# Performance work log

Measured on AMD Instinct MI355X. Metric: run time of the kernel, lower is better.

Reference implementation:

```python
import jax, jax.numpy as jnp
import numpy as np

# FrictionConfig constants (chosen in init_kwargs)
K_STEPS = 4
ETA = 0.1
ETA_DECAY = 0.9
MU_MAX = 10.0
SMOOTH_LAMBDA = 0.1
RADIUS = 8
B, S, H = 4, 2048, 1024
INNER = max(H // 2, 32)  # 512


def _build_window_edges(length, radius):
    chunks = []
    for d in range(1, radius + 1):
        i = np.arange(length - d, dtype=np.int32)
        chunks.append(np.stack([i, i + d], axis=1))
    return np.concatenate(chunks, axis=0)  # [E, 2]


def setup_inputs() -> dict:
    key = jax.random.key(0)
    ks = jax.random.split(key, 8)
    hidden = jax.random.normal(ks[0], (B, S, H), dtype=jnp.float32)
    attention_mask = jnp.ones((B, S), dtype=jnp.int32)
    edges = jnp.asarray(_build_window_edges(S, RADIUS))
    # edge_mlp: Linear(2, INNER) -> GELU -> Linear(INNER, 1)
    W1 = jax.random.normal(ks[1], (2, INNER), dtype=jnp.float32) * (1.0 / np.sqrt(2))
    b1 = jnp.zeros((INNER,), dtype=jnp.float32)
    W2 = jax.random.normal(ks[2], (INNER, 1), dtype=jnp.float32) * (1.0 / np.sqrt(INNER))
    b2 = jnp.zeros((1,), dtype=jnp.float32)
    # q_proj: Linear(H, H)
    Wq = jax.random.normal(ks[3], (H, H), dtype=jnp.float32) * (1.0 / np.sqrt(H))
    bq = jnp.zeros((H,), dtype=jnp.float32)
    # LayerNorm
    gamma = jnp.ones((H,), dtype=jnp.float32)
    beta = jnp.zeros((H,), dtype=jnp.float32)
    return {"hidden": hidden, "attention_mask": attention_mask, "edges": edges,
            "Wq": Wq, "bq": bq, "W1": W1, "b1": b1, "W2": W2, "b2": b2,
            "gamma": gamma, "beta": beta}


def _edge_weights(h, ei, ej, W1, b1, W2, b2):
    hi = h[ei]  # [E, H]
    hj = h[ej]
    diff = hi - hj
    dist = jnp.linalg.norm(diff, axis=-1, keepdims=True)           # [E, 1]
    ni = jnp.maximum(jnp.linalg.norm(hi, axis=-1), 1e-6)
    nj = jnp.maximum(jnp.linalg.norm(hj, axis=-1), 1e-6)
    cos = (jnp.sum(hi * hj, axis=-1) / (ni * nj))[:, None]         # [E, 1]
    feats = jnp.concatenate([dist, cos], axis=-1)                  # [E, 2]
    z = jax.nn.gelu(feats @ W1 + b1, approximate=False) @ W2 + b2  # [E, 1]
    return jax.nn.softplus(z) + 1e-5


def _laplacian(h, ei, ej, mu):
    n = h.shape[0]
    weighted = mu * (h[ei] - h[ej])  # [E, H]
    # normalize_laplacian = True
    w = mu[:, 0]
    deg = jnp.zeros((n,), h.dtype).at[ei].add(w).at[ej].add(w)
    inv_sqrt = jnp.maximum(deg, 1e-6) ** -0.5
    weighted = weighted * (inv_sqrt[ei] * inv_sqrt[ej])[:, None]
    lap = jnp.zeros_like(h).at[ei].add(weighted).at[ej].add(-weighted)
    return lap


def _smooth(s):
    left = jnp.concatenate([s[:1], s[:-1]], axis=0)
    right = jnp.concatenate([s[1:], s[-1:]], axis=0)
    return s - SMOOTH_LAMBDA * (2.0 * s - left - right)


def _layernorm(x, gamma, beta):
    m = x.mean(axis=-1, keepdims=True)
    v = x.var(axis=-1, keepdims=True)
    return (x - m) * jax.lax.rsqrt(v + 1e-5) * gamma + beta


def _run_single(h, ei, ej, Wq, bq, W1, b1, W2, b2, gamma, beta):
    q = h @ Wq + bq
    state = h
    mu = None
    for step in range(K_STEPS):
        mu = _edge_weights(state, ei, ej, W1, b1, W2, b2)  # recompute_mu=True
        mu = jnp.minimum(mu, MU_MAX)
        lap = _laplacian(state, ei, ej, mu)
        eta = ETA * (ETA_DECAY ** step)
        state = state - eta * (lap - q)
        state = _smooth(state)
    out = _layernorm(state + h, gamma, beta)
    diffs = state[ei] - state[ej]
    energy = 0.5 * jnp.sum(mu[:, 0] * jnp.sum(diffs * diffs, axis=-1))
    return out, energy


def reference(hidden, attention_mask, edges, Wq, bq, W1, b1, W2, b2, gamma, beta):
    # All masks are full-length, so edges are identical across batch and
    # the outer Python batch loop vectorizes to a vmap.
    ei, ej = edges[:, 0], edges[:, 1]
    outputs, energy = jax.vmap(
        lambda h: _run_single(h, ei, ej, Wq, bq, W1, b1, W2, b2, gamma, beta)
    )(hidden)
    return outputs, energy
```

## Files before the change

### kernel.cpp

```cpp
#include <hip/hip_runtime.h>

#define BB 4
#define SS 2048
#define HH 1024
#define TQ 32
#define TU 32
#define CW 256

typedef unsigned short u16;
typedef __bf16 bf16x8 __attribute__((ext_vector_type(8)));
typedef float f32x4 __attribute__((ext_vector_type(4)));

__device__ __forceinline__ float b2f(u16 u){
  union { unsigned int i; float f; } v; v.i = ((unsigned int)u) << 16; return v.f;
}
__device__ __forceinline__ u16 f2b(float f){
  union { float f; unsigned int i; } v; v.f = f;
  unsigned int x = v.i;
  return (u16)((x + 0x7fffu + ((x >> 16) & 1u)) >> 16);
}
__device__ __forceinline__ float4 u4f(ushort4 v){
  float4 o; o.x = b2f(v.x); o.y = b2f(v.y); o.z = b2f(v.z); o.w = b2f(v.w); return o;
}
__device__ __forceinline__ ushort4 f4u(float4 v){
  ushort4 o; o.x = f2b(v.x); o.y = f2b(v.y); o.z = f2b(v.z); o.w = f2b(v.w); return o;
}
__device__ __forceinline__ float wave_sum(float v){
  #pragma unroll
  for(int m = 32; m > 0; m >>= 1) v += __shfl_xor(v, m);
  return v;
}
__device__ __forceinline__ float pread(const void* p, int i, int f){
  return f ? b2f(((const u16*)p)[i]) : ((const float*)p)[i];
}
__device__ __forceinline__ void gload16(const void* g, void* l){
  __builtin_amdgcn_global_load_lds((const __attribute__((address_space(1))) unsigned int*)g,
                                   (__attribute__((address_space(3))) unsigned int*)l, 16, 0, 0);
}
__device__ __forceinline__ float fast_gelu(float z){
  float x  = z * 0.70710678118654752f;
  float ax = fabsf(x);
  float t  = __builtin_amdgcn_rcpf(fmaf(0.3275911f, ax, 1.f));
  float poly = ((((1.061405429f*t - 1.453152027f)*t + 1.421413741f)*t
                 - 0.284496736f)*t + 0.254829592f)*t;
  float er = fmaf(-poly, __expf(-ax*ax), 1.f);
  er = (x < 0.f) ? -er : er;
  return 0.5f*z*(1.f + er);
}

__global__ __launch_bounds__(256) void k_params(const void* bq, const void* W1, const void* b1,
                                                const void* W2, const void* b2, const void* gm,
                                                const void* bt, float* bqc, float* W1c, float* b1c,
                                                float* W2c, float* b2c, float* gmc, float* btc,
                                                int* flagp){
  __shared__ int sf;
  if(threadIdx.x == 0){
    int f = (((const u16*)gm)[0] == 0x3F80u) ? 1 : 0;
    sf = f; *flagp = f;
  }
  __syncthreads();
  int f = sf, t = threadIdx.x;
  for(int i = t; i < 1024; i += 256) bqc[i] = pread(bq, i, f);
  for(int i = t; i < 1024; i += 256) W1c[i] = pread(W1, i, f);
  for(int i = t; i <  512; i += 256) b1c[i] = pread(b1, i, f);
  for(int i = t; i <  512; i += 256) W2c[i] = pread(W2, i, f);
  if(t == 0) b2c[0] = pread(b2, 0, f);
  for(int i = t; i < 1024; i += 256) gmc[i] = pread(gm, i, f);
  for(int i = t; i < 1024; i += 256) btc[i] = pread(bt, i, f);
}

__global__ __launch_bounds__(256) void k_cvt(const void* h, u16* s, const int* flagp){
  int f = *flagp;
  size_t i4 = (size_t)blockIdx.x*256 + threadIdx.x;
  if(f){
    ((ushort4*)s)[i4] = ((const ushort4*)h)[i4];
  } else {
    float4 v = ((const float4*)h)[i4];
    ((ushort4*)s)[i4] = f4u(v);
  }
}

__global__ __launch_bounds__(256) void k_transpose(const void* W, u16* __restrict__ Wt,
                                                   const int* flagp){
  int f = *flagp;
  __shared__ u16 t[32][33];
  int bx = blockIdx.x, by = blockIdx.y;
  int tx = threadIdx.x, ty = threadIdx.y;
  #pragma unroll
  for(int r = 0; r < 32; r += 8){
    int idx = (by*32 + ty + r)*HH + bx*32 + tx;
    float v = f ? b2f(((const u16*)W)[idx]) : ((const float*)W)[idx];
    t[ty + r][tx] = f2b(v);
  }
  __syncthreads();
  #pragma unroll
  for(int r = 0; r < 32; r += 8)
    Wt[(size_t)(bx*32 + ty + r)*HH + by*32 + tx] = t[tx][ty + r];
}

__global__ __launch_bounds__(256) void k_qgemm(const u16* __restrict__ A, const u16* __restrict__ Wt,
                                               const float* __restrict__ bqc, u16* __restrict__ q){
  __shared__ u16 lA[128*32];
  __shared__ u16 lB[128*32];
  int m0 = blockIdx.x*128, n0 = blockIdx.y*128;
  int tid  = threadIdx.x;
  int wave = tid >> 6, lane = tid & 63;
  int wm = (wave >> 1)*64, wn = (wave & 1)*64;
  int quad = lane >> 4, l16 = lane & 15;
  int srow = tid >> 2;
  int scol = (tid & 3)*8;

  f32x4 acc[4][4];
  #pragma unroll
  for(int i = 0; i < 4; i++)
    #pragma unroll
    for(int j = 0; j < 4; j++) acc[i][j] = (f32x4){0.f,0.f,0.f,0.f};

  for(int k0 = 0; k0 < HH; k0 += 32){
    __syncthreads();
    gload16(A  + (size_t)(m0 + srow     )*HH + k0 + scol, &lA[ srow     *32 + scol]);
    gload16(A  + (size_t)(m0 + srow + 64)*HH + k0 + scol, &lA[(srow+64) *32 + scol]);
    gload16(Wt + (size_t)(n0 + srow     )*HH + k0 + scol, &lB[ srow     *32 + scol]);
    gload16(Wt + (size_t)(n0 + srow + 64)*HH + k0 + scol, &lB[(srow+64) *32 + scol]);
    __syncthreads();
    bf16x8 af[4];
    #pragma unroll
    for(int mt = 0; mt < 4; mt++)
      af[mt] = *(const bf16x8*)&lA[(wm + mt*16 + l16)*32 + quad*8];
    #pragma unroll
    for(int nt = 0; nt < 4; nt++){
      bf16x8 bf = *(const bf16x8*)&lB[(wn + nt*16 + l16)*32 + quad*8];
      #pragma unroll
      for(int mt = 0; mt < 4; mt++)
        acc[mt][nt] = __builtin_amdgcn_mfma_f32_16x16x32_bf16(af[mt], bf, acc[mt][nt], 0, 0, 0);
    }
  }
  #pragma unroll
  for(int nt = 0; nt < 4; nt++){
    int col = n0 + wn + nt*16 + l16;
    float bqv = bqc[col];
    #pragma unroll
    for(int mt = 0; mt < 4; mt++){
      #pragma unroll
      for(int r = 0; r < 4; r++){
        int row = m0 + wm + mt*16 + quad*4 + r;
        q[(size_t)row*HH + col] = f2b(acc[mt][nt][r] + bqv);
      }
    }
  }
}

__global__ __launch_bounds__(512) void k_gram_mu(const u16* __restrict__ s,
                                                 const float* __restrict__ W1c, const float* __restrict__ b1c,
                                                 const float* __restrict__ W2c, const float* __restrict__ b2c,
                                                 float* __restrict__ mu){
  __shared__ float Gband[40*9];
  __shared__ float4 wpk[512];
  int b = blockIdx.y, i0 = blockIdx.x*TQ;
  int tid = threadIdx.x, wave = tid >> 6, lane = tid & 63;

  if(tid < 512) wpk[tid] = make_float4(W1c[tid], W1c[512+tid], b1c[tid], W2c[tid]);

  if(wave < 4){
    int ti = wave >> 1;
    int tj = (wave + 1) >> 1;
    int quad = lane >> 4, l16 = lane & 15;
    int ra = i0 + ti*16 + l16; if(ra > SS-1) ra = SS-1;
    int rb = i0 + tj*16 + l16; if(rb > SS-1) rb = SS-1;
    const u16* ar = s + ((size_t)b*SS + ra)*HH + quad*8;
    const u16* br = s + ((size_t)b*SS + rb)*HH + quad*8;
    f32x4 acc = (f32x4){0.f,0.f,0.f,0.f};
    #pragma unroll 8
    for(int k0 = 0; k0 < HH; k0 += 32){
      bf16x8 af = *(const bf16x8*)(ar + k0);
      bf16x8 bf = *(const bf16x8*)(br + k0);
      acc = __builtin_amdgcn_mfma_f32_16x16x32_bf16(af, bf, acc, 0, 0, 0);
    }
    #pragma unroll
    for(int r = 0; r < 4; r++){
      int gr = ti*16 + quad*4 + r;
      int dd = tj*16 + l16 - gr;
      if(dd >= 0 && dd <= 8) Gband[gr*9 + dd] = acc[r];
    }
  } else {
    for(int rr = wave - 4; rr < 8; rr += 4){
      int r = 32 + rr;
      int row = i0 + r; if(row > SS-1) row = SS-1;
      const ushort4* rp = (const ushort4*)(s + ((size_t)b*SS + row)*HH);
      float a = 0.f;
      #pragma unroll
      for(int c = 0; c < 4; c++){
        float4 v = u4f(rp[lane + 64*c]);
        a += v.x*v.x + v.y*v.y + v.z*v.z + v.w*v.w;
      }
      a = wave_sum(a);
      if(lane == 0) Gband[r*9] = a;
    }
  }
  __syncthreads();

  int e = tid >> 1, h = tid & 1;
  int d = (e >> 5) + 1, k = e & 31;
  bool valid = (i0 + k + d) < SS;
  float gii = Gband[k*9], gjj = Gband[(k+d)*9], gij = Gband[k*9 + d];
  float dist = sqrtf(fmaxf(gii + gjj - 2.f*gij, 0.f));
  float ni = fmaxf(sqrtf(gii), 1e-6f);
  float nj = fmaxf(sqrtf(gjj), 1e-6f);
  float cosv = gij * __builtin_amdgcn_rcpf(ni * nj);
  float acc = 0.f;
  const float4* wp = &wpk[h*256];
  #pragma unroll 4
  for(int j0 = 0; j0 < 256; j0++){
    float4 wv = wp[j0];
    float z1 = fmaf(dist, wv.x, fmaf(cosv, wv.y, wv.z));
    acc = fmaf(fast_gelu(z1), wv.w, acc);
  }
  acc += __shfl_xor(acc, 1);
  if(h == 0 && valid){
    float z  = acc + b2c[0];
    float sp = fmaxf(z, 0.f) + __logf(1.f + __expf(-fabsf(z)));
    mu[((size_t)b*8 + (d-1))*SS + (i0 + k)] = fminf(sp + 1e-5f, 10.0f);
  }
}

__global__ __launch_bounds__(256) void k_upsm(const u16* __restrict__ sIn, u16* __restrict__ sOut,
                                              const u16* __restrict__ q, const float* __restrict__ mu,
                                              float eta){
  __shared__ u16 st[50*CW];
  __shared__ u16 up[34*CW];
  __shared__ float invsS[50];
  __shared__ float muS[58*8];
  int i0 = blockIdx.x*TU, c0 = blockIdx.y*CW, b = blockIdx.z;
  int tid = threadIdx.x;

  for(int idx = tid; idx < 58*8; idx += 256){
    int ir = idx >> 3, d = (idx & 7) + 1;
    int i = i0 - 17 + ir;
    float v = 0.f;
    if(i >= 0 && i + d < SS) v = mu[((size_t)b*8 + d-1)*SS + i];
    muS[idx] = v;
  }
  for(int idx = tid; idx < 50*(CW/4); idx += 256){
    int r = idx / (CW/4), cc = idx % (CW/4);
    int i = i0 - 9 + r;
    ushort4 v = {0,0,0,0};
    if(i >= 0 && i < SS) v = *(const ushort4*)(sIn + ((size_t)b*SS + i)*HH + c0 + cc*4);
    ((ushort4*)st)[idx] = v;
  }
  __syncthreads();
  if(tid < 50){
    int ir = tid + 8;
    float deg = 0.f;
    #pragma unroll
    for(int d = 1; d <= 8; d++){
      deg += muS[ir*8 + d-1];
      deg += muS[(ir-d)*8 + d-1];
    }
    invsS[tid] = 1.0f / sqrtf(fmaxf(deg, 1e-6f));
  }
  __syncthreads();

  int rq = tid >> 6, lane = tid & 63;
  for(int jr = 0; jr < 9; jr++){
    int r = rq + jr*4;
    if(r >= 34) break;
    int i = i0 - 1 + r;
    if(i < 0 || i >= SS) continue;
    int sr = r + 8, vr = r + 8, mr = r + 16;
    float inv_i = invsS[vr];
    float4 si = u4f(((const ushort4*)(st + (size_t)sr*CW))[lane]);
    float A = 0.f;
    float4 acc = {0.f,0.f,0.f,0.f};
    #pragma unroll
    for(int d = 1; d <= 8; d++){
      float cR = muS[mr*8 + d-1]     * inv_i        * invsS[vr+d];
      float cL = muS[(mr-d)*8 + d-1] * invsS[vr-d]  * inv_i;
      A += cR + cL;
      float4 vR = u4f(((const ushort4*)(st + (size_t)(sr+d)*CW))[lane]);
      float4 vL = u4f(((const ushort4*)(st + (size_t)(sr-d)*CW))[lane]);
      acc.x -= cR*vR.x + cL*vL.x; acc.y -= cR*vR.y + cL*vL.y;
      acc.z -= cR*vR.z + cL*vL.z; acc.w -= cR*vR.w + cL*vL.w;
    }
    acc.x += A*si.x; acc.y += A*si.y; acc.z += A*si.z; acc.w += A*si.w;
    float4 qv = u4f(*(const ushort4*)(q + ((size_t)b*SS + i)*HH + c0 + lane*4));
    float4 o;
    o.x = si.x - eta*(acc.x - qv.x);
    o.y = si.y - eta*(acc.y - qv.y);
    o.z = si.z - eta*(acc.z - qv.z);
    o.w = si.w - eta*(acc.w - qv.w);
    ((ushort4*)(up + (size_t)r*CW))[lane] = f4u(o);
  }
  __syncthreads();
  for(int js = 0; js < 8; js++){
    int rr = rq + js*4;
    int i = i0 + rr;
    int ur = rr + 1;
    float4 c  = u4f(((const ushort4*)(up + (size_t)ur*CW))[lane]);
    float4 l  = (i > 0)      ? u4f(((const ushort4*)(up + (size_t)(ur-1)*CW))[lane]) : c;
    float4 r4 = (i < SS-1)   ? u4f(((const ushort4*)(up + (size_t)(ur+1)*CW))[lane]) : c;
    float4 o;
    o.x = c.x - 0.1f*(2.f*c.x - l.x - r4.x);
    o.y = c.y - 0.1f*(2.f*c.y - l.y - r4.y);
    o.z = c.z - 0.1f*(2.f*c.z - l.z - r4.z);
    o.w = c.w - 0.1f*(2.f*c.w - l.w - r4.w);
    *(ushort4*)(sOut + ((size_t)b*SS + i)*HH + c0 + lane*4) = f4u(o);
  }
}

__global__ __launch_bounds__(256) void k_out(const u16* __restrict__ sA, const void* __restrict__ hraw,
                                             const float* __restrict__ gmc, const float* __restrict__ btc,
                                             void* __restrict__ outp, const int* flagp){
  int f = *flagp;
  int b = blockIdx.x >> 11, i = blockIdx.x & (SS-1);
  int tid = threadIdx.x;
  size_t row = (size_t)b*SS + i;
  float4 sv = u4f(((const ushort4*)(sA + row*HH))[tid]);
  float4 hv;
  if(f) hv = u4f(((const ushort4*)((const u16*)hraw + row*HH))[tid]);
  else  hv = ((const float4*)((const float*)hraw + row*HH))[tid];
  float x0 = sv.x + hv.x, x1 = sv.y + hv.y, x2 = sv.z + hv.z, x3 = sv.w + hv.w;

  __shared__ float sh[4];
  int wv = tid >> 6, lane = tid & 63;
  float lsum = wave_sum(x0 + x1 + x2 + x3);
  if(lane == 0) sh[wv] = lsum;
  __syncthreads();
  float mean = (sh[0] + sh[1] + sh[2] + sh[3]) * (1.f/HH);
  __syncthreads();
  float d0 = x0-mean, d1 = x1-mean, d2 = x2-mean, d3 = x3-mean;
  float lsq = wave_sum(d0*d0 + d1*d1 + d2*d2 + d3*d3);
  if(lane == 0) sh[wv] = lsq;
  __syncthreads();
  float var = (sh[0] + sh[1] + sh[2] + sh[3]) * (1.f/HH);
  float sc = 1.0f / sqrtf(var + 1e-5f);

  int col = tid*4;
  float4 o;
  o.x = d0*sc*gmc[col+0] + btc[col+0];
  o.y = d1*sc*gmc[col+1] + btc[col+1];
  o.z = d2*sc*gmc[col+2] + btc[col+2];
  o.w = d3*sc*gmc[col+3] + btc[col+3];
  if(f) ((ushort4*)((u16*)outp + row*HH))[tid] = f4u(o);
  else  ((float4*)((float*)outp + row*HH))[tid] = o;
}

__global__ __launch_bounds__(512) void k_energy(const u16* __restrict__ s, const float* __restrict__ mu,
                                                float* __restrict__ partials){
  __shared__ float Gband[40*9];
  __shared__ float wacc[8];
  int b = blockIdx.y, i0 = blockIdx.x*TQ;
  int tid = threadIdx.x, wave = tid >> 6, lane = tid & 63;

  if(wave < 4){
    int ti = wave >> 1;
    int tj = (wave + 1) >> 1;
    int quad = lane >> 4, l16 = lane & 15;
    int ra = i0 + ti*16 + l16; if(ra > SS-1) ra = SS-1;
    int rb = i0 + tj*16 + l16; if(rb > SS-1) rb = SS-1;
    const u16* ar = s + ((size_t)b*SS + ra)*HH + quad*8;
    const u16* br = s + ((size_t)b*SS + rb)*HH + quad*8;
    f32x4 acc = (f32x4){0.f,0.f,0.f,0.f};
    #pragma unroll 8
    for(int k0 = 0; k0 < HH; k0 += 32){
      bf16x8 af = *(const bf16x8*)(ar + k0);
      bf16x8 bf = *(const bf16x8*)(br + k0);
      acc = __builtin_amdgcn_mfma_f32_16x16x32_bf16(af, bf, acc, 0, 0, 0);
    }
    #pragma unroll
    for(int r = 0; r < 4; r++){
      int gr = ti*16 + quad*4 + r;
      int dd = tj*16 + l16 - gr;
      if(dd >= 0 && dd <= 8) Gband[gr*9 + dd] = acc[r];
    }
  } else {
    for(int rr = wave - 4; rr < 8; rr += 4){
      int r = 32 + rr;
      int row = i0 + r; if(row > SS-1) row = SS-1;
      const ushort4* rp = (const ushort4*)(s + ((size_t)b*SS + row)*HH);
      float a = 0.f;
      #pragma unroll
      for(int c = 0; c < 4; c++){
        float4 v = u4f(rp[lane + 64*c]);
        a += v.x*v.x + v.y*v.y + v.z*v.z + v.w*v.w;
      }
      a = wave_sum(a);
      if(lane == 0) Gband[r*9] = a;
    }
  }
  __syncthreads();

  int d = wave + 1;
  int k = lane;
  float esum = 0.f;
  if(k < 32 && (i0 + k + d) < SS){
    float d2 = fmaxf(Gband[k*9] + Gband[(k+d)*9] - 2.f*Gband[k*9 + d], 0.f);
    esum = mu[((size_t)b*8 + (d-1))*SS + (i0 + k)] * d2;
  }
  esum = wave_sum(esum);
  if(lane == 0) wacc[wave] = esum;
  __syncthreads();
  if(tid == 0){
    float t = 0.f;
    #pragma unroll
    for(int w2 = 0; w2 < 8; w2++) t += wacc[w2];
    partials[(size_t)b*64 + blockIdx.x] = t;
  }
}

__global__ __launch_bounds__(64) void k_efinal(const float* __restrict__ partials, void* __restrict__ outp,
                                               const int* flagp){
  int f = *flagp;
  int b = blockIdx.x;
  float sacc = partials[(size_t)b*64 + threadIdx.x];
  sacc = wave_sum(sacc);
  if(threadIdx.x == 0){
    float e = 0.5f * sacc;
    if(f) ((u16*)outp)[(size_t)BB*SS*HH + b] = f2b(e);
    else  ((float*)outp)[(size_t)BB*SS*HH + b] = e;
  }
}

extern "C" void kernel_launch(void* const* d_in, const int* in_sizes, int n_in,
                              void* d_out, int out_size, void* d_ws, size_t ws_size,
                              hipStream_t stream) {
  const void* hidden = d_in[0];
  const void* Wq  = d_in[3];
  const void* bq  = d_in[4];
  const void* W1  = d_in[5];
  const void* b1  = d_in[6];
  const void* W2  = d_in[7];
  const void* b2v = d_in[8];
  const void* gamma = d_in[9];
  const void* beta  = d_in[10];

  char* w = (char*)d_ws;
  u16*   q   = (u16*)w;   w += (size_t)BB*SS*HH*2;
  u16*   sA  = (u16*)w;   w += (size_t)BB*SS*HH*2;
  u16*   Wt  = (u16*)w;   w += (size_t)HH*HH*2;
  float* mu  = (float*)w; w += (size_t)BB*8*SS*4;
  float* partials = (float*)w; w += (size_t)BB*64*4;
  float* bqc = (float*)w; w += 1024*4;
  float* W1c = (float*)w; w += 1024*4;
  float* b1c = (float*)w; w += 512*4;
  float* W2c = (float*)w; w += 512*4;
  float* b2c = (float*)w; w += 4;
  float* gmc = (float*)w; w += 1024*4;
  float* btc = (float*)w; w += 1024*4;
  int*   flagp = (int*)w; w += 4;
  u16* sB = (u16*)d_out;

  k_params   <<<1, 256, 0, stream>>>(bq, W1, b1, W2, b2v, gamma, beta,
                                     bqc, W1c, b1c, W2c, b2c, gmc, btc, flagp);
  k_cvt      <<<(BB*SS*HH/4)/256, 256, 0, stream>>>(hidden, sA, flagp);
  k_transpose<<<dim3(HH/32, HH/32), dim3(32,8), 0, stream>>>(Wq, Wt, flagp);
  k_qgemm    <<<dim3(BB*SS/128, HH/128), 256, 0, stream>>>(sA, Wt, bqc, q);

  const float etas[4] = {0.1f, 0.09f, 0.081f, 0.0729f};
  for(int step = 0; step < 4; step++){
    const u16* cur = (step & 1) ? sB : sA;
    u16*       nxt = (step & 1) ? sA : sB;
    k_gram_mu<<<dim3(SS/TQ, BB), 512, 0, stream>>>(cur, W1c, b1c, W2c, b2c, mu);
    k_upsm   <<<dim3(SS/TU, HH/CW, BB), 256, 0, stream>>>(cur, nxt, q, mu, etas[step]);
  }
  k_out   <<<BB*SS, 256, 0, stream>>>(sA, hidden, gmc, btc, d_out, flagp);
  k_energy<<<dim3(SS/TQ, BB), 512, 0, stream>>>(sA, mu, partials);
  k_efinal<<<BB, 64, 0, stream>>>(partials, d_out, flagp);
}
```

Before: 406.0 us.

## Fuse setup kernels, split gram_mu edges, register-pipeline upsm smoothing, fuse energy reduction

Merges the param, convert and transpose kernels into one launch and folds the final energy reduction into k_energy with atomics and a last-block counter. This removes three kernel launches. k_gram_mu now splits the 8 distances across two blocks and uses 4 lanes per edge. It folds the 1/sqrt2 scale into the weights and simplifies the GELU algebra. k_upsm drops the shared up buffer and applies the 3-tap smoothing from a rolling register window. That saves LDS and a barrier but recomputes two halo rows per wave group.

```diff
diff --git a/kernel.cpp b/kernel.cpp
--- a/kernel.cpp
+++ b/kernel.cpp
@@ -33,69 +33,56 @@
 __device__ __forceinline__ float pread(const void* p, int i, int f){
   return f ? b2f(((const u16*)p)[i]) : ((const float*)p)[i];
 }
+__device__ __forceinline__ int dflag(const void* gm){
+  return (((const u16*)gm)[0] == 0x3F80u) ? 1 : 0;
+}
 __device__ __forceinline__ void gload16(const void* g, void* l){
   __builtin_amdgcn_global_load_lds((const __attribute__((address_space(1))) unsigned int*)g,
                                    (__attribute__((address_space(3))) unsigned int*)l, 16, 0, 0);
 }
-__device__ __forceinline__ float fast_gelu(float z){
-  float x  = z * 0.70710678118654752f;
-  float ax = fabsf(x);
-  float t  = __builtin_amdgcn_rcpf(fmaf(0.3275911f, ax, 1.f));
-  float poly = ((((1.061405429f*t - 1.453152027f)*t + 1.421413741f)*t
-                 - 0.284496736f)*t + 0.254829592f)*t;
-  float er = fmaf(-poly, __expf(-ax*ax), 1.f);
-  er = (x < 0.f) ? -er : er;
-  return 0.5f*z*(1.f + er);
-}
-
-__global__ __launch_bounds__(256) void k_params(const void* bq, const void* W1, const void* b1,
-                                                const void* W2, const void* b2, const void* gm,
-                                                const void* bt, float* bqc, float* W1c, float* b1c,
-                                                float* W2c, float* b2c, float* gmc, float* btc,
-                                                int* flagp){
-  __shared__ int sf;
-  if(threadIdx.x == 0){
-    int f = (((const u16*)gm)[0] == 0x3F80u) ? 1 : 0;
-    sf = f; *flagp = f;
-  }
-  __syncthreads();
-  int f = sf, t = threadIdx.x;
-  for(int i = t; i < 1024; i += 256) bqc[i] = pread(bq, i, f);
-  for(int i = t; i < 1024; i += 256) W1c[i] = pread(W1, i, f);
-  for(int i = t; i <  512; i += 256) b1c[i] = pread(b1, i, f);
-  for(int i = t; i <  512; i += 256) W2c[i] = pread(W2, i, f);
-  if(t == 0) b2c[0] = pread(b2, 0, f);
-  for(int i = t; i < 1024; i += 256) gmc[i] = pread(gm, i, f);
-  for(int i = t; i < 1024; i += 256) btc[i] = pread(bt, i, f);
-}
-
-__global__ __launch_bounds__(256) void k_cvt(const void* h, u16* s, const int* flagp){
-  int f = *flagp;
-  size_t i4 = (size_t)blockIdx.x*256 + threadIdx.x;
-  if(f){
-    ((ushort4*)s)[i4] = ((const ushort4*)h)[i4];
+
+__global__ __launch_bounds__(256) void k_setup(const void* hidden, u16* __restrict__ s,
+                                               const void* Wq, u16* __restrict__ Wt,
+                                               const void* bq, const void* W1, const void* b1,
+                                               const void* W2, const void* b2, const void* gm,
+                                               const void* bt,
+                                               float* bqc, float* W1c, float* b1c, float* W2c,
+                                               float* b2c, float* gmc, float* btc,
+                                               float* partials, int* ecnt){
+  __shared__ u16 t[32][33];
+  int f = dflag(gm);
+  int bid = blockIdx.x, tid = threadIdx.x;
+  if(bid < 8192){
+    size_t i4 = (size_t)bid*256 + tid;
+    if(f){
+      ((ushort4*)s)[i4] = ((const ushort4*)hidden)[i4];
+    } else {
+      ((ushort4*)s)[i4] = f4u(((const float4*)hidden)[i4]);
+    }
+  } else if(bid < 8192 + 1024){
+    int bi = bid - 8192;
+    int bx = bi & 31, by = bi >> 5;
+    int tx = tid & 31, ty = tid >> 5;
+    #pragma unroll
+    for(int r = 0; r < 32; r += 8){
+      int idx = (by*32 + ty + r)*HH + bx*32 + tx;
+      float v = f ? b2f(((const u16*)Wq)[idx]) : ((const float*)Wq)[idx];
+      t[ty + r][tx] = f2b(v);
+    }
+    __syncthreads();
+    #pragma unroll
+    for(int r = 0; r < 32; r += 8)
+      Wt[(size_t)(bx*32 + ty + r)*HH + by*32 + tx] = t[tx][ty + r];
   } else {
-    float4 v = ((const float4*)h)[i4];
-    ((ushort4*)s)[i4] = f4u(v);
-  }
-}
-
-__global__ __launch_bounds__(256) void k_transpose(const void* W, u16* __restrict__ Wt,
-                                                   const int* flagp){
-  int f = *flagp;
-  __shared__ u16 t[32][33];
-  int bx = blockIdx.x, by = blockIdx.y;
-  int tx = threadIdx.x, ty = threadIdx.y;
-  #pragma unroll
-  for(int r = 0; r < 32; r += 8){
-    int idx = (by*32 + ty + r)*HH + bx*32 + tx;
-    float v = f ? b2f(((const u16*)W)[idx]) : ((const float*)W)[idx];
-    t[ty + r][tx] = f2b(v);
-  }
-  __syncthreads();
-  #pragma unroll
-  for(int r = 0; r < 32; r += 8)
-    Wt[(size_t)(bx*32 + ty + r)*HH + by*32 + tx] = t[tx][ty + r];
+    for(int i = tid; i < 1024; i += 256) bqc[i] = pread(bq, i, f);
+    for(int i = tid; i < 1024; i += 256) W1c[i] = pread(W1, i, f);
+    for(int i = tid; i <  512; i += 256) b1c[i] = pread(b1, i, f);
+    for(int i = tid; i <  512; i += 256) W2c[i] = pread(W2, i, f);
+    if(tid == 0) b2c[0] = pread(b2, 0, f);
+    for(int i = tid; i < 1024; i += 256) gmc[i] = pread(gm, i, f);
+    for(int i = tid; i < 1024; i += 256) btc[i] = pread(bt, i, f);
+    if(tid < BB){ partials[tid] = 0.f; ecnt[tid] = 0; }
+  }
 }
 
 __global__ __launch_bounds__(256) void k_qgemm(const u16* __restrict__ A, const u16* __restrict__ Wt,
@@ -156,10 +143,13 @@
                                                  float* __restrict__ mu){
   __shared__ float Gband[40*9];
   __shared__ float4 wpk[512];
-  int b = blockIdx.y, i0 = blockIdx.x*TQ;
+  int b = blockIdx.z, i0 = blockIdx.x*TQ;
   int tid = threadIdx.x, wave = tid >> 6, lane = tid & 63;
 
-  if(tid < 512) wpk[tid] = make_float4(W1c[tid], W1c[512+tid], b1c[tid], W2c[tid]);
+  wpk[tid] = make_float4(W1c[tid]     * 0.70710678118654752f,
+                         W1c[512+tid] * 0.70710678118654752f,
+                         b1c[tid]     * 0.70710678118654752f,
+                         W2c[tid]     * 0.70710678118654752f);
 
   if(wave < 4){
     int ti = wave >> 1;
@@ -199,8 +189,9 @@
   }
   __syncthreads();
 
-  int e = tid >> 1, h = tid & 1;
-  int d = (e >> 5) + 1, k = e & 31;
+  int el = tid >> 2, qd = tid & 3;
+  int dl = el >> 5, k = el & 31;
+  int d = blockIdx.y*4 + dl + 1;
   bool valid = (i0 + k + d) < SS;
   float gii = Gband[k*9], gjj = Gband[(k+d)*9], gij = Gband[k*9 + d];
   float dist = sqrtf(fmaxf(gii + gjj - 2.f*gij, 0.f));
@@ -208,26 +199,31 @@
   float nj = fmaxf(sqrtf(gjj), 1e-6f);
   float cosv = gij * __builtin_amdgcn_rcpf(ni * nj);
   float acc = 0.f;
-  const float4* wp = &wpk[h*256];
+  const float4* wp = &wpk[qd*128];
   #pragma unroll 4
-  for(int j0 = 0; j0 < 256; j0++){
+  for(int j0 = 0; j0 < 128; j0++){
     float4 wv = wp[j0];
-    float z1 = fmaf(dist, wv.x, fmaf(cosv, wv.y, wv.z));
-    acc = fmaf(fast_gelu(z1), wv.w, acc);
+    float x  = fmaf(dist, wv.x, fmaf(cosv, wv.y, wv.z));
+    float ax = fabsf(x);
+    float t  = __builtin_amdgcn_rcpf(fmaf(0.3275911f, ax, 1.f));
+    float poly = ((((1.061405429f*t - 1.453152027f)*t + 1.421413741f)*t
+                   - 0.284496736f)*t + 0.254829592f)*t;
+    float ape = ax * poly * __expf(-ax*ax);
+    acc = fmaf(x + ax - ape, wv.w, acc);
   }
   acc += __shfl_xor(acc, 1);
-  if(h == 0 && valid){
+  acc += __shfl_xor(acc, 2);
+  if(qd == 0 && valid){
     float z  = acc + b2c[0];
     float sp = fmaxf(z, 0.f) + __logf(1.f + __expf(-fabsf(z)));
     mu[((size_t)b*8 + (d-1))*SS + (i0 + k)] = fminf(sp + 1e-5f, 10.0f);
   }
 }
 
-__global__ __launch_bounds__(256) void k_upsm(const u16* __restrict__ sIn, u16* __restrict__ sOut,
-                                              const u16* __restrict__ q, const float* __restrict__ mu,
-                                              float eta){
+__global__ __launch_bounds__(256, 4) void k_upsm(const u16* __restrict__ sIn, u16* __restrict__ sOut,
+                                                 const u16* __restrict__ q, const float* __restrict__ mu,
+                                                 float eta){
   __shared__ u16 st[50*CW];
-  __shared__ u16 up[34*CW];
   __shared__ float invsS[50];
   __shared__ float muS[58*8];
   int i0 = blockIdx.x*TU, c0 = blockIdx.y*CW, b = blockIdx.z;
@@ -261,56 +257,56 @@
   __syncthreads();
 
   int rq = tid >> 6, lane = tid & 63;
-  for(int jr = 0; jr < 9; jr++){
-    int r = rq + jr*4;
-    if(r >= 34) break;
-    int i = i0 - 1 + r;
-    if(i < 0 || i >= SS) continue;
-    int sr = r + 8, vr = r + 8, mr = r + 16;
-    float inv_i = invsS[vr];
-    float4 si = u4f(((const ushort4*)(st + (size_t)sr*CW))[lane]);
-    float A = 0.f;
-    float4 acc = {0.f,0.f,0.f,0.f};
-    #pragma unroll
-    for(int d = 1; d <= 8; d++){
-      float cR = muS[mr*8 + d-1]     * inv_i        * invsS[vr+d];
-      float cL = muS[(mr-d)*8 + d-1] * invsS[vr-d]  * inv_i;
-      A += cR + cL;
-      float4 vR = u4f(((const ushort4*)(st + (size_t)(sr+d)*CW))[lane]);
-      float4 vL = u4f(((const ushort4*)(st + (size_t)(sr-d)*CW))[lane]);
-      acc.x -= cR*vR.x + cL*vL.x; acc.y -= cR*vR.y + cL*vL.y;
-      acc.z -= cR*vR.z + cL*vL.z; acc.w -= cR*vR.w + cL*vL.w;
-    }
-    acc.x += A*si.x; acc.y += A*si.y; acc.z += A*si.z; acc.w += A*si.w;
-    float4 qv = u4f(*(const ushort4*)(q + ((size_t)b*SS + i)*HH + c0 + lane*4));
-    float4 o;
-    o.x = si.x - eta*(acc.x - qv.x);
-    o.y = si.y - eta*(acc.y - qv.y);
-    o.z = si.z - eta*(acc.z - qv.z);
-    o.w = si.w - eta*(acc.w - qv.w);
-    ((ushort4*)(up + (size_t)r*CW))[lane] = f4u(o);
-  }
-  __syncthreads();
-  for(int js = 0; js < 8; js++){
-    int rr = rq + js*4;
-    int i = i0 + rr;
-    int ur = rr + 1;
-    float4 c  = u4f(((const ushort4*)(up + (size_t)ur*CW))[lane]);
-    float4 l  = (i > 0)      ? u4f(((const ushort4*)(up + (size_t)(ur-1)*CW))[lane]) : c;
-    float4 r4 = (i < SS-1)   ? u4f(((const ushort4*)(up + (size_t)(ur+1)*CW))[lane]) : c;
-    float4 o;
-    o.x = c.x - 0.1f*(2.f*c.x - l.x - r4.x);
-    o.y = c.y - 0.1f*(2.f*c.y - l.y - r4.y);
-    o.z = c.z - 0.1f*(2.f*c.z - l.z - r4.z);
-    o.w = c.w - 0.1f*(2.f*c.w - l.w - r4.w);
-    *(ushort4*)(sOut + ((size_t)b*SS + i)*HH + c0 + lane*4) = f4u(o);
+  float4 ua = {0,0,0,0}, ub = {0,0,0,0}, uc = {0,0,0,0};
+  #pragma unroll
+  for(int k = 0; k < 10; k++){
+    int ur = rq*8 + k;
+    int i  = i0 - 1 + ur;
+    float4 o = {0.f,0.f,0.f,0.f};
+    if(i >= 0 && i < SS){
+      int sr = ur + 8, vr = ur + 8, mr = ur + 16;
+      float inv_i = invsS[vr];
+      float4 si = u4f(((const ushort4*)(st + (size_t)sr*CW))[lane]);
+      float A = 0.f;
+      float4 acc = {0.f,0.f,0.f,0.f};
+      #pragma unroll
+      for(int d = 1; d <= 8; d++){
+        float cR = muS[mr*8 + d-1]     * inv_i        * invsS[vr+d];
+        float cL = muS[(mr-d)*8 + d-1] * invsS[vr-d]  * inv_i;
+        A += cR + cL;
+        float4 vR = u4f(((const ushort4*)(st + (size_t)(sr+d)*CW))[lane]);
+        float4 vL = u4f(((const ushort4*)(st + (size_t)(sr-d)*CW))[lane]);
+        acc.x -= cR*vR.x + cL*vL.x; acc.y -= cR*vR.y + cL*vL.y;
+        acc.z -= cR*vR.z + cL*vL.z; acc.w -= cR*vR.w + cL*vL.w;
+      }
+      acc.x += A*si.x; acc.y += A*si.y; acc.z += A*si.z; acc.w += A*si.w;
+      float4 qv = u4f(*(const ushort4*)(q + ((size_t)b*SS + i)*HH + c0 + lane*4));
+      o.x = si.x - eta*(acc.x - qv.x);
+      o.y = si.y - eta*(acc.y - qv.y);
+      o.z = si.z - eta*(acc.z - qv.z);
+      o.w = si.w - eta*(acc.w - qv.w);
+    }
+    ua = ub; ub = uc; uc = o;
+    if(k >= 2){
+      int rr = rq*8 + k - 2;
+      int iout = i0 + rr;
+      float4 cc2 = ub;
+      float4 l  = (iout > 0)     ? ua : cc2;
+      float4 r4 = (iout < SS-1)  ? uc : cc2;
+      float4 oo;
+      oo.x = cc2.x - 0.1f*(2.f*cc2.x - l.x - r4.x);
+      oo.y = cc2.y - 0.1f*(2.f*cc2.y - l.y - r4.y);
+      oo.z = cc2.z - 0.1f*(2.f*cc2.z - l.z - r4.z);
+      oo.w = cc2.w - 0.1f*(2.f*cc2.w - l.w - r4.w);
+      *(ushort4*)(sOut + ((size_t)b*SS + iout)*HH + c0 + lane*4) = f4u(oo);
+    }
   }
 }
 
 __global__ __launch_bounds__(256) void k_out(const u16* __restrict__ sA, const void* __restrict__ hraw,
                                              const float* __restrict__ gmc, const float* __restrict__ btc,
-                                             void* __restrict__ outp, const int* flagp){
-  int f = *flagp;
+                                             void* __restrict__ outp, const void* __restrict__ gmraw){
+  int f = dflag(gmraw);
   int b = blockIdx.x >> 11, i = blockIdx.x & (SS-1);
   int tid = threadIdx.x;
   size_t row = (size_t)b*SS + i;
@@ -345,7 +341,8 @@
 }
 
 __global__ __launch_bounds__(512) void k_energy(const u16* __restrict__ s, const float* __restrict__ mu,
-                                                float* __restrict__ partials){
+                                                float* __restrict__ partials, int* __restrict__ ecnt,
+                                                const void* __restrict__ gmraw, void* __restrict__ outp){
   __shared__ float Gband[40*9];
   __shared__ float wacc[8];
   int b = blockIdx.y, i0 = blockIdx.x*TQ;
@@ -403,20 +400,16 @@
     float t = 0.f;
     #pragma unroll
     for(int w2 = 0; w2 < 8; w2++) t += wacc[w2];
-    partials[(size_t)b*64 + blockIdx.x] = t;
-  }
-}
-
-__global__ __launch_bounds__(64) void k_efinal(const float* __restrict__ partials, void* __restrict__ outp,
-                                               const int* flagp){
-  int f = *flagp;
-  int b = blockIdx.x;
-  float sacc = partials[(size_t)b*64 + threadIdx.x];
-  sacc = wave_sum(sacc);
-  if(threadIdx.x == 0){
-    float e = 0.5f * sacc;
-    if(f) ((u16*)outp)[(size_t)BB*SS*HH + b] = f2b(e);
-    else  ((float*)outp)[(size_t)BB*SS*HH + b] = e;
+    atomicAdd(&partials[b], t);
+    __threadfence();
+    int old = atomicAdd(&ecnt[b], 1);
+    if(old == (SS/TQ) - 1){
+      float tot = atomicAdd(&partials[b], 0.0f);
+      float e = 0.5f * tot;
+      int f = dflag(gmraw);
+      if(f) ((u16*)outp)[(size_t)BB*SS*HH + b] = f2b(e);
+      else  ((float*)outp)[(size_t)BB*SS*HH + b] = e;
+    }
   }
 }
 
@@ -438,7 +431,8 @@
   u16*   sA  = (u16*)w;   w += (size_t)BB*SS*HH*2;
   u16*   Wt  = (u16*)w;   w += (size_t)HH*HH*2;
   float* mu  = (float*)w; w += (size_t)BB*8*SS*4;
-  float* partials = (float*)w; w += (size_t)BB*64*4;
+  float* partials = (float*)w; w += BB*4;
+  int*   ecnt = (int*)w;  w += BB*4;
   float* bqc = (float*)w; w += 1024*4;
   float* W1c = (float*)w; w += 1024*4;
   float* b1c = (float*)w; w += 512*4;
@@ -446,23 +440,20 @@
   float* b2c = (float*)w; w += 4;
   float* gmc = (float*)w; w += 1024*4;
   float* btc = (float*)w; w += 1024*4;
-  int*   flagp = (int*)w; w += 4;
   u16* sB = (u16*)d_out;
 
-  k_params   <<<1, 256, 0, stream>>>(bq, W1, b1, W2, b2v, gamma, beta,
-                                     bqc, W1c, b1c, W2c, b2c, gmc, btc, flagp);
-  k_cvt      <<<(BB*SS*HH/4)/256, 256, 0, stream>>>(hidden, sA, flagp);
-  k_transpose<<<dim3(HH/32, HH/32), dim3(32,8), 0, stream>>>(Wq, Wt, flagp);
-  k_qgemm    <<<dim3(BB*SS/128, HH/128), 256, 0, stream>>>(sA, Wt, bqc, q);
+  k_setup<<<8192 + 1024 + 1, 256, 0, stream>>>(hidden, sA, Wq, Wt, bq, W1, b1, W2, b2v,
+                                               gamma, beta, bqc, W1c, b1c, W2c, b2c, gmc, btc,
+                                               partials, ecnt);
+  k_qgemm<<<dim3(BB*SS/128, HH/128), 256, 0, stream>>>(sA, Wt, bqc, q);
 
   const float etas[4] = {0.1f, 0.09f, 0.081f, 0.0729f};
   for(int step = 0; step < 4; step++){
     const u16* cur = (step & 1) ? sB : sA;
     u16*       nxt = (step & 1) ? sA : sB;
-    k_gram_mu<<<dim3(SS/TQ, BB), 512, 0, stream>>>(cur, W1c, b1c, W2c, b2c, mu);
+    k_gram_mu<<<dim3(SS/TQ, 2, BB), 512, 0, stream>>>(cur, W1c, b1c, W2c, b2c, mu);
     k_upsm   <<<dim3(SS/TU, HH/CW, BB), 256, 0, stream>>>(cur, nxt, q, mu, etas[step]);
   }
-  k_out   <<<BB*SS, 256, 0, stream>>>(sA, hidden, gmc, btc, d_out, flagp);
-  k_energy<<<dim3(SS/TQ, BB), 512, 0, stream>>>(sA, mu, partials);
-  k_efinal<<<BB, 64, 0, stream>>>(partials, d_out, flagp);
-}
+  k_out   <<<BB*SS, 256, 0, stream>>>(sA, hidden, gmc, btc, d_out, gamma);
+  k_energy<<<dim3(SS/TQ, BB), 512, 0, stream>>>(sA, mu, partials, ecnt, gamma, d_out);
+}
```

Result: no change. 402.1 us (-0.9%).
